# Kernel optimization log

Measured on AMD Instinct MI355X. Metric: run time of the kernel, lower is better.

Reference implementation:

```python
import jax, jax.numpy as jnp
import numpy as np
import math

B, T, C = 8, 2048, 1024
DIM_ATT, DIM_FFN = 1024, 4096
N_LAYER, LAYER_ID = 12, 1
EPS = 1e-5


def setup_inputs() -> dict:
    key = jax.random.key(0)
    ks = jax.random.split(key, 16)

    # deterministic init constants per RWKV source
    r01 = LAYER_ID / (N_LAYER - 1)
    r1a0 = 1.0 - LAYER_ID / N_LAYER
    ddd = (np.arange(C, dtype=np.float32) / C)[None, None, :]
    decay_speed = -5.0 + 8.0 * (np.arange(DIM_ATT, dtype=np.float32) / (DIM_ATT - 1)) ** (0.7 + 1.3 * r01)
    zigzag = (np.array([(i + 1) % 3 - 1 for i in range(DIM_ATT)], dtype=np.float32)) * 0.5

    def lin(k, out_d, in_d):
        return jax.random.normal(k, (out_d, in_d), jnp.float32) * (1.0 / math.sqrt(in_d))

    return {
        "x": jax.random.normal(ks[0], (B, T, C), jnp.float32),
        "ln1_w": jnp.ones((C,), jnp.float32),
        "ln1_b": jnp.zeros((C,), jnp.float32),
        "ln2_w": jnp.ones((C,), jnp.float32),
        "ln2_b": jnp.zeros((C,), jnp.float32),
        # time-mix (attention) params
        "att_tmk": jnp.asarray(ddd ** r1a0),
        "att_tmv": jnp.asarray(ddd ** r1a0 + 0.3 * r01),
        "att_tmr": jnp.asarray(ddd ** (0.5 * r1a0)),
        "time_decay": jnp.asarray(decay_speed),
        "time_first": jnp.asarray(np.full(DIM_ATT, math.log(0.3), np.float32) + zigzag),
        "Wk": lin(ks[1], DIM_ATT, C),
        "Wv": lin(ks[2], DIM_ATT, C),
        "Wr": lin(ks[3], DIM_ATT, C),
        "Wo": lin(ks[4], C, DIM_ATT),
        # channel-mix params
        "ffn_tmk": jnp.asarray(ddd ** r1a0),
        "ffn_tmr": jnp.asarray(ddd ** r1a0),
        "Wkey": lin(ks[5], DIM_FFN, C),
        "Wrec": lin(ks[6], C, C),
        "Wval": lin(ks[7], C, DIM_FFN),
    }


def layer_norm(x, w, b):
    mu = jnp.mean(x, axis=-1, keepdims=True)
    var = jnp.mean(jnp.square(x - mu), axis=-1, keepdims=True)
    return (x - mu) * jax.lax.rsqrt(var + EPS) * w + b


def time_shift(x):
    # xx[:, t] = x[:, t-1], zero at t=0  (nn.ZeroPad2d((0,0,1,-1)))
    return jnp.pad(x, ((0, 0), (1, 0), (0, 0)))[:, :-1, :]


def wkv(time_decay, time_first, k, v):
    # numerically stable RWKV-4 WKV recurrence, vectorized over (B, C)
    w = -jnp.exp(time_decay)  # [C]
    u = time_first            # [C]

    def step(carry, kv_t):
        aa, bb, pp = carry        # each [B, C]
        kt, vt = kv_t             # [B, C]
        ww = u + kt
        qq = jnp.maximum(pp, ww)
        e1 = jnp.exp(pp - qq)
        e2 = jnp.exp(ww - qq)
        y = (e1 * aa + e2 * vt) / (e1 * bb + e2)
        ww2 = pp + w
        qq2 = jnp.maximum(ww2, kt)
        e1b = jnp.exp(ww2 - qq2)
        e2b = jnp.exp(kt - qq2)
        return (e1b * aa + e2b * vt, e1b * bb + e2b, qq2), y

    init = (jnp.zeros_like(k[:, 0]), jnp.zeros_like(k[:, 0]),
            jnp.full_like(k[:, 0], -1e38))
    kT = jnp.swapaxes(k, 0, 1)  # [T, B, C]
    vT = jnp.swapaxes(v, 0, 1)
    _, yT = jax.lax.scan(step, init, (kT, vT))
    return jnp.swapaxes(yT, 0, 1)  # [B, T, C]


def reference(x, ln1_w, ln1_b, ln2_w, ln2_b,
              att_tmk, att_tmv, att_tmr, time_decay, time_first,
              Wk, Wv, Wr, Wo,
              ffn_tmk, ffn_tmr, Wkey, Wrec, Wval):
    # --- time-mix (attention) with residual ---
    h = layer_norm(x, ln1_w, ln1_b)
    hh = time_shift(h)
    xk = h * att_tmk + hh * (1 - att_tmk)
    xv = h * att_tmv + hh * (1 - att_tmv)
    xr = h * att_tmr + hh * (1 - att_tmr)
    k = xk @ Wk.T
    v = xv @ Wv.T
    sr = jax.nn.sigmoid(xr @ Wr.T)
    rwkv = sr * wkv(time_decay, time_first, k, v)
    x = x + rwkv @ Wo.T

    # --- channel-mix (FFN) with residual ---
    h = layer_norm(x, ln2_w, ln2_b)
    hh = time_shift(h)
    xk = h * ffn_tmk + hh * (1 - ffn_tmk)
    xr = h * ffn_tmr + hh * (1 - ffn_tmr)
    kk = jnp.square(jax.nn.relu(xk @ Wkey.T))
    kv = kk @ Wval.T
    x = x + jax.nn.sigmoid(xr @ Wrec.T) * kv
    return x
```

## Files before the change

### kernel.cpp

```cpp
#include <hip/hip_runtime.h>
#include <stdint.h>

#define B_ 8
#define T_ 2048
#define C_ 1024
#define F_ 4096
#define M_ (B_*T_)
#define NC 16
#define LCH (T_/NC)

typedef __attribute__((ext_vector_type(8))) short bf16x8;
typedef __attribute__((ext_vector_type(4))) float f32x4;

static __device__ __forceinline__ unsigned short f2bf(float f) {
    union { float f; unsigned u; } v; v.f = f;
    unsigned r = v.u + 0x7fffu + ((v.u >> 16) & 1u);
    return (unsigned short)(r >> 16);
}
static __device__ __forceinline__ float bf2f(unsigned short h) {
    union { unsigned u; float f; } v; v.u = ((unsigned)h) << 16;
    return v.f;
}

#define GLDS16(gp, lp) __builtin_amdgcn_global_load_lds( \
    (const __attribute__((address_space(1))) unsigned int*)(gp), \
    (__attribute__((address_space(3))) unsigned int*)(lp), 16, 0, 0)

#define SB0() __builtin_amdgcn_sched_barrier(0)
#define MFMA_BF16(a, b, c) __builtin_amdgcn_mfma_f32_16x16x32_bf16((a), (b), (c), 0, 0, 0)

struct WSrc { const float* p[7]; };

__global__ __launch_bounds__(256) void k_convert(WSrc w, unsigned short* __restrict__ dst) {
    size_t e = ((size_t)blockIdx.x * 256 + threadIdx.x) * 4;
    int seg = (int)(e >> 20);
    const float* s; size_t off;
    if (seg < 5)      { s = w.p[seg]; off = e - ((size_t)seg << 20); }
    else if (seg < 9) { s = w.p[5];   off = e - (5ull << 20); }
    else              { s = w.p[6];   off = e - (9ull << 20); }
    float4 v = *(const float4*)(s + off);
    ushort4 o;
    o.x = f2bf(v.x); o.y = f2bf(v.y); o.z = f2bf(v.z); o.w = f2bf(v.w);
    *(ushort4*)(dst + e) = o;
}

template<int THREE>
__global__ __launch_bounds__(256) void k_ln_mix(
    const float* __restrict__ xin, const float* __restrict__ lw, const float* __restrict__ lb,
    const float* __restrict__ tk, const float* __restrict__ tv, const float* __restrict__ tr,
    unsigned short* __restrict__ ok, unsigned short* __restrict__ ov, unsigned short* __restrict__ orr)
{
    __shared__ float sred[4][4];
    const int m = blockIdx.x;
    const int t = m & (T_ - 1);
    const int tid = threadIdx.x;
    const int col0 = tid * 4;

    const float4 xc = *(const float4*)(xin + (size_t)m * C_ + col0);
    float4 xp = make_float4(0.f, 0.f, 0.f, 0.f);
    if (t > 0) xp = *(const float4*)(xin + (size_t)(m - 1) * C_ + col0);

    float s1 = xc.x + xc.y + xc.z + xc.w;
    float s2 = xc.x*xc.x + xc.y*xc.y + xc.z*xc.z + xc.w*xc.w;
    float s3 = xp.x + xp.y + xp.z + xp.w;
    float s4 = xp.x*xp.x + xp.y*xp.y + xp.z*xp.z + xp.w*xp.w;
    #pragma unroll
    for (int off = 32; off > 0; off >>= 1) {
        s1 += __shfl_down(s1, off);
        s2 += __shfl_down(s2, off);
        s3 += __shfl_down(s3, off);
        s4 += __shfl_down(s4, off);
    }
    const int wave = tid >> 6, lane = tid & 63;
    if (lane == 0) { sred[0][wave]=s1; sred[1][wave]=s2; sred[2][wave]=s3; sred[3][wave]=s4; }
    __syncthreads();
    const float S1 = sred[0][0]+sred[0][1]+sred[0][2]+sred[0][3];
    const float S2 = sred[1][0]+sred[1][1]+sred[1][2]+sred[1][3];
    const float S3 = sred[2][0]+sred[2][1]+sred[2][2]+sred[2][3];
    const float S4 = sred[3][0]+sred[3][1]+sred[3][2]+sred[3][3];

    const float inv = 1.0f / (float)C_;
    const float muc = S1 * inv;
    const float rc  = rsqrtf(S2 * inv - muc * muc + 1e-5f);
    const float mup = S3 * inv;
    const float rp  = rsqrtf(S4 * inv - mup * mup + 1e-5f);

    const float xcv[4] = {xc.x, xc.y, xc.z, xc.w};
    const float xpv[4] = {xp.x, xp.y, xp.z, xp.w};
    unsigned short rk[4], rv[4], rr[4];
    #pragma unroll
    for (int i = 0; i < 4; ++i) {
        const int col = col0 + i;
        const float w_ = lw[col], b_ = lb[col];
        const float h  = (xcv[i] - muc) * rc * w_ + b_;
        const float hh = (t > 0) ? (xpv[i] - mup) * rp * w_ + b_ : 0.f;
        const float ak = tk[col];
        rk[i] = f2bf(h * ak + hh * (1.f - ak));
        if (THREE) { const float av = tv[col]; rv[i] = f2bf(h * av + hh * (1.f - av)); }
        const float ar = tr[col];
        rr[i] = f2bf(h * ar + hh * (1.f - ar));
    }
    const size_t o = (size_t)m * C_ + col0;
    ushort4 u;
    u.x = rk[0]; u.y = rk[1]; u.z = rk[2]; u.w = rk[3];
    *(ushort4*)(ok + o) = u;
    if (THREE) {
        u.x = rv[0]; u.y = rv[1]; u.z = rv[2]; u.w = rv[3];
        *(ushort4*)(ov + o) = u;
    }
    u.x = rr[0]; u.y = rr[1]; u.z = rr[2]; u.w = rr[3];
    *(ushort4*)(orr + o) = u;
}

__global__ __launch_bounds__(256) void k_wkv_local(
    const unsigned short* __restrict__ kb, const unsigned short* __restrict__ vb,
    const float* __restrict__ tdec, float4* __restrict__ st)
{
    const int g = blockIdx.x * 256 + threadIdx.x;
    const int c = g & (C_ - 1);
    const int j = (g >> 10) & (NC - 1);
    const int b = g >> 14;
    const float w = -__expf(tdec[c]);
    float aa = 0.f, bb = 0.f, pp = -1e38f;
    const size_t base = ((size_t)(b * T_ + j * LCH)) * C_ + c;
    #pragma unroll 4
    for (int t = 0; t < LCH; ++t) {
        const float kt = bf2f(kb[base + (size_t)t * C_]);
        const float vt = bf2f(vb[base + (size_t)t * C_]);
        const float ww2 = pp + w;
        const float qq2 = fmaxf(ww2, kt);
        const float e1b = __expf(ww2 - qq2);
        const float e2b = __expf(kt - qq2);
        aa = e1b * aa + e2b * vt;
        bb = e1b * bb + e2b;
        pp = qq2;
    }
    st[((size_t)b * NC + j) * C_ + c] = make_float4(aa, bb, pp, 0.f);
}

__global__ __launch_bounds__(256) void k_wkv_scan(
    const unsigned short* __restrict__ kb, const unsigned short* __restrict__ vb,
    const unsigned short* __restrict__ sr,
    const float* __restrict__ tdec, const float* __restrict__ tfirst,
    const float4* __restrict__ st, unsigned short* __restrict__ p)
{
    const int g = blockIdx.x * 256 + threadIdx.x;
    const int c = g & (C_ - 1);
    const int j = (g >> 10) & (NC - 1);
    const int b = g >> 14;
    const float w = -__expf(tdec[c]);
    const float u = tfirst[c];

    float aa = 0.f, bb = 0.f, pp = -1e38f;
    for (int i = 0; i < j; ++i) {
        const float4 s = st[((size_t)b * NC + i) * C_ + c];
        const float pdec = pp + w * (float)LCH;
        const float q  = fmaxf(pdec, s.z);
        const float eA = __expf(pdec - q);
        const float eB = __expf(s.z - q);
        aa = eA * aa + eB * s.x;
        bb = eA * bb + eB * s.y;
        pp = q;
    }

    const size_t base = ((size_t)(b * T_ + j * LCH)) * C_ + c;
    #pragma unroll 4
    for (int t = 0; t < LCH; ++t) {
        const size_t idx = base + (size_t)t * C_;
        const float kt = bf2f(kb[idx]);
        const float vt = bf2f(vb[idx]);
        const float ww = u + kt;
        const float qq = fmaxf(pp, ww);
        const float e1 = __expf(pp - qq);
        const float e2 = __expf(ww - qq);
        const float y  = (e1 * aa + e2 * vt) / (e1 * bb + e2);
        p[idx] = f2bf(bf2f(sr[idx]) * y);
        const float ww2 = pp + w;
        const float qq2 = fmaxf(ww2, kt);
        const float e1b = __expf(ww2 - qq2);
        const float e2b = __expf(kt - qq2);
        aa = e1b * aa + e2b * vt;
        bb = e1b * bb + e2b;
        pp = qq2;
    }
}

static __device__ __forceinline__ void gemm_core256(
    const unsigned short* __restrict__ A, int lda,
    const unsigned short* __restrict__ Bw, int ldb,
    int K, int m0, int n0,
    unsigned short* As, unsigned short* Bs, f32x4 acc[8][4])
{
    const int tid  = threadIdx.x;
    const int l    = tid & 63;
    const int l16  = l & 15, quad = l >> 4;
    const int w    = tid >> 6;
    const int wm   = w >> 2, wn = w & 3;

    const int sr_ = tid >> 3;
    const int sb_ = (tid & 7) ^ (sr_ & 7);
    const unsigned short* gA = A  + (size_t)(m0 + sr_) * lda + sb_ * 8;
    const unsigned short* gB = Bw + (size_t)(n0 + sr_) * ldb + sb_ * 8;

    auto stA = [&](int tt, int ss, int u) {
        GLDS16(gA + (size_t)u * 64 * lda + tt * 64, As + ss * 16384 + u * 4096 + w * 512);
    };
    auto stB = [&](int tt, int ss, int u) {
        GLDS16(gB + (size_t)u * 64 * ldb + tt * 64, Bs + ss * 16384 + u * 4096 + w * 512);
    };

    const int swz = l16 & 7;
    const unsigned short* aR = As + (wm * 128 + l16) * 64;
    const unsigned short* bR = Bs + (wn * 64  + l16) * 64;
    const int o0 = ((0 + quad) ^ swz) * 8;
    const int o1 = ((4 + quad) ^ swz) * 8;

    stA(0, 0, 0); stA(0, 0, 2);
    stB(0, 0, 0); stB(0, 0, 1); stB(0, 0, 2); stB(0, 0, 3);
    stA(0, 0, 1); stA(0, 0, 3);
    asm volatile("s_waitcnt vmcnt(0)" ::: "memory");
    SB0();
    __builtin_amdgcn_s_barrier();
    SB0();

    const int NT = K >> 6;
    for (int t = 0; t < NT; ++t) {
        const int rs = t & 1, ns = rs ^ 1;
        const unsigned short* ab = aR + rs * 16384;
        const unsigned short* bb = bR + rs * 16384;
        const bool pf = (t + 1 < NT);
        bf16x8 b0[4], b1[4];

        {
            bf16x8 a0[2], a1[2];
            #pragma unroll
            for (int j = 0; j < 4; ++j) {
                b0[j] = *(const bf16x8*)(bb + j * 1024 + o0);
                b1[j] = *(const bf16x8*)(bb + j * 1024 + o1);
            }
            #pragma unroll
            for (int i = 0; i < 2; ++i) {
                a0[i] = *(const bf16x8*)(ab + i * 1024 + o0);
                a1[i] = *(const bf16x8*)(ab + i * 1024 + o1);
            }
            if (pf) { stA(t + 1, ns, 0); stA(t + 1, ns, 2); }
            SB0();
            __builtin_amdgcn_s_barrier();
            asm volatile("s_waitcnt lgkmcnt(0)" ::: "memory");
            SB0();
            __builtin_amdgcn_s_setprio(1);
            #pragma unroll
            for (int i = 0; i < 2; ++i)
                #pragma unroll
                for (int j = 0; j < 4; ++j) {
                    acc[i][j] = MFMA_BF16(a0[i], b0[j], acc[i][j]);
                    acc[i][j] = MFMA_BF16(a1[i], b1[j], acc[i][j]);
                }
            __builtin_amdgcn_s_setprio(0);
            SB0();
            __builtin_amdgcn_s_barrier();
            SB0();
        }

        {
            bf16x8 a0[2], a1[2];
            #pragma unroll
            for (int i = 0; i < 2; ++i) {
                a0[i] = *(const bf16x8*)(ab + (2 + i) * 1024 + o0);
                a1[i] = *(const bf16x8*)(ab + (2 + i) * 1024 + o1);
            }
            if (pf) { stB(t + 1, ns, 0); stB(t + 1, ns, 1); stB(t + 1, ns, 2); stB(t + 1, ns, 3); }
            SB0();
            __builtin_amdgcn_s_barrier();
            asm volatile("s_waitcnt lgkmcnt(0)" ::: "memory");
            SB0();
            __builtin_amdgcn_s_setprio(1);
            #pragma unroll
            for (int i = 0; i < 2; ++i)
                #pragma unroll
                for (int j = 0; j < 4; ++j) {
                    acc[2 + i][j] = MFMA_BF16(a0[i], b0[j], acc[2 + i][j]);
                    acc[2 + i][j] = MFMA_BF16(a1[i], b1[j], acc[2 + i][j]);
                }
            __builtin_amdgcn_s_setprio(0);
            asm volatile("s_waitcnt vmcnt(6)" ::: "memory");
            SB0();
            __builtin_amdgcn_s_barrier();
            SB0();
        }

        {
            bf16x8 a0[2], a1[2];
            #pragma unroll
            for (int i = 0; i < 2; ++i) {
                a0[i] = *(const bf16x8*)(ab + (4 + i) * 1024 + o0);
                a1[i] = *(const bf16x8*)(ab + (4 + i) * 1024 + o1);
            }
            if (pf) { stA(t + 1, ns, 1); stA(t + 1, ns, 3); }
            SB0();
            __builtin_amdgcn_s_barrier();
            asm volatile("s_waitcnt lgkmcnt(0)" ::: "memory");
            SB0();
            __builtin_amdgcn_s_setprio(1);
            #pragma unroll
            for (int i = 0; i < 2; ++i)
                #pragma unroll
                for (int j = 0; j < 4; ++j) {
                    acc[4 + i][j] = MFMA_BF16(a0[i], b0[j], acc[4 + i][j]);
                    acc[4 + i][j] = MFMA_BF16(a1[i], b1[j], acc[4 + i][j]);
                }
            __builtin_amdgcn_s_setprio(0);
            SB0();
            __builtin_amdgcn_s_barrier();
            SB0();
        }

        {
            bf16x8 a0[2], a1[2];
            #pragma unroll
            for (int i = 0; i < 2; ++i) {
                a0[i] = *(const bf16x8*)(ab + (6 + i) * 1024 + o0);
                a1[i] = *(const bf16x8*)(ab + (6 + i) * 1024 + o1);
            }
            SB0();
            __builtin_amdgcn_s_barrier();
            asm volatile("s_waitcnt lgkmcnt(0)" ::: "memory");
            SB0();
            __builtin_amdgcn_s_setprio(1);
            #pragma unroll
            for (int i = 0; i < 2; ++i)
                #pragma unroll
                for (int j = 0; j < 4; ++j) {
                    acc[6 + i][j] = MFMA_BF16(a0[i], b0[j], acc[6 + i][j]);
                    acc[6 + i][j] = MFMA_BF16(a1[i], b1[j], acc[6 + i][j]);
                }
            __builtin_amdgcn_s_setprio(0);
            asm volatile("s_waitcnt vmcnt(2)" ::: "memory");
            SB0();
            __builtin_amdgcn_s_barrier();
            SB0();
        }
    }
}

template<int EPI>
__global__ __launch_bounds__(512, 1) void k_gemm(
    const unsigned short* __restrict__ A, int lda,
    const unsigned short* __restrict__ Bw, int ldb,
    int K, int N,
    float* __restrict__ outF, unsigned short* __restrict__ outH,
    const float* __restrict__ resid, const unsigned short* __restrict__ mul)
{
    __shared__ unsigned short As[2 * 16384];
    __shared__ unsigned short Bs[2 * 16384];
    f32x4 acc[8][4];
    const f32x4 zero = {0.f, 0.f, 0.f, 0.f};
    #pragma unroll
    for (int i = 0; i < 8; ++i)
        #pragma unroll
        for (int j = 0; j < 4; ++j) acc[i][j] = zero;

    const int m0 = blockIdx.x * 256, n0 = blockIdx.y * 256;
    gemm_core256(A, lda, Bw, ldb, K, m0, n0, As, Bs, acc);

    const int lane = threadIdx.x & 63, wave = threadIdx.x >> 6;
    const int quad = lane >> 4, l16 = lane & 15;
    const int wm = (wave >> 2) * 128, wn = (wave & 3) * 64;
    #pragma unroll
    for (int i = 0; i < 8; ++i) {
        const int rowb = m0 + wm + i * 16 + quad * 4;
        #pragma unroll
        for (int j = 0; j < 4; ++j) {
            const int col = n0 + wn + j * 16 + l16;
            #pragma unroll
            for (int r = 0; r < 4; ++r) {
                const size_t idx = (size_t)(rowb + r) * N + col;
                const float v = acc[i][j][r];
                if (EPI == 1)      outH[idx] = f2bf(1.f / (1.f + __expf(-v)));
                else if (EPI == 2) outF[idx] = resid[idx] + v;
                else if (EPI == 3) { const float z = v > 0.f ? v : 0.f; outH[idx] = f2bf(z * z); }
                else               outF[idx] = outF[idx] + bf2f(mul[idx]) * v;
            }
        }
    }
}

__global__ __launch_bounds__(512, 1) void k_gemm_kvr(
    const unsigned short* __restrict__ xk, const unsigned short* __restrict__ xv,
    const unsigned short* __restrict__ xr,
    const unsigned short* __restrict__ W3,
    unsigned short* __restrict__ ok, unsigned short* __restrict__ ov,
    unsigned short* __restrict__ orr)
{
    __shared__ unsigned short As[2 * 16384];
    __shared__ unsigned short Bs[2 * 16384];
    f32x4 acc[8][4];
    const f32x4 zero = {0.f, 0.f, 0.f, 0.f};
    #pragma unroll
    for (int i = 0; i < 8; ++i)
        #pragma unroll
        for (int j = 0; j < 4; ++j) acc[i][j] = zero;

    const int m0 = blockIdx.x * 256, n0 = blockIdx.y * 256;
    const int seg = n0 >> 10;
    const unsigned short* A = (seg == 0) ? xk : (seg == 1) ? xv : xr;
    unsigned short* outH    = (seg == 0) ? ok : (seg == 1) ? ov : orr;

    gemm_core256(A, C_, W3, C_, C_, m0, n0, As, Bs, acc);

    const int nl0 = n0 & (C_ - 1);
    const int lane = threadIdx.x & 63, wave = threadIdx.x >> 6;
    const int quad = lane >> 4, l16 = lane & 15;
    const int wm = (wave >> 2) * 128, wn = (wave & 3) * 64;
    #pragma unroll
    for (int i = 0; i < 8; ++i) {
        const int rowb = m0 + wm + i * 16 + quad * 4;
        #pragma unroll
        for (int j = 0; j < 4; ++j) {
            const int col = nl0 + wn + j * 16 + l16;
            #pragma unroll
            for (int r = 0; r < 4; ++r) {
                const size_t idx = (size_t)(rowb + r) * C_ + col;
                float v = acc[i][j][r];
                if (seg == 2) v = 1.f / (1.f + __expf(-v));
                outH[idx] = f2bf(v);
            }
        }
    }
}

extern "C" void kernel_launch(void* const* d_in, const int* in_sizes, int n_in,
                              void* d_out, int out_size, void* d_ws, size_t ws_size,
                              hipStream_t stream)
{
    const float* x      = (const float*)d_in[0];
    const float* ln1w   = (const float*)d_in[1];
    const float* ln1b   = (const float*)d_in[2];
    const float* ln2w   = (const float*)d_in[3];
    const float* ln2b   = (const float*)d_in[4];
    const float* atk    = (const float*)d_in[5];
    const float* atv    = (const float*)d_in[6];
    const float* atr    = (const float*)d_in[7];
    const float* tdec   = (const float*)d_in[8];
    const float* tfirst = (const float*)d_in[9];
    const float* Wk     = (const float*)d_in[10];
    const float* Wv     = (const float*)d_in[11];
    const float* Wr     = (const float*)d_in[12];
    const float* Wo     = (const float*)d_in[13];
    const float* ftk    = (const float*)d_in[14];
    const float* ftr    = (const float*)d_in[15];
    const float* Wkey   = (const float*)d_in[16];
    const float* Wrec   = (const float*)d_in[17];
    const float* Wval   = (const float*)d_in[18];
    float* out = (float*)d_out;

    char* ws = (char*)d_ws;
    const size_t MB = 1ull << 20;
    unsigned short* xk  = (unsigned short*)(ws + 0 * MB);
    unsigned short* xv  = (unsigned short*)(ws + 32 * MB);
    unsigned short* xr  = (unsigned short*)(ws + 64 * MB);
    unsigned short* sr  = (unsigned short*)(ws + 96 * MB);
    unsigned short* wb  = (unsigned short*)(ws + 128 * MB);
    float4* states      = (float4*)(ws + 0 * MB);
    unsigned short* p   = xv;
    unsigned short* xk2 = xk;
    unsigned short* xr2 = xr;
    unsigned short* s2  = sr;
    unsigned short* tmp = xv;
    unsigned short* kb  = (unsigned short*)d_out;
    unsigned short* vb  = (unsigned short*)d_out + (32*MB/2);

    unsigned short* W3_b   = wb;
    unsigned short* Wo_b   = wb + 3 * (1u << 20);
    unsigned short* Wrec_b = wb + 4 * (1u << 20);
    unsigned short* Wkey_b = wb + 5 * (1u << 20);
    unsigned short* Wval_b = wb + 9 * (1u << 20);

    WSrc wsrc; wsrc.p[0]=Wk; wsrc.p[1]=Wv; wsrc.p[2]=Wr; wsrc.p[3]=Wo;
    wsrc.p[4]=Wrec; wsrc.p[5]=Wkey; wsrc.p[6]=Wval;
    k_convert<<<dim3(13312), dim3(256), 0, stream>>>(wsrc, wb);

    k_ln_mix<1><<<dim3(M_), dim3(256), 0, stream>>>(x, ln1w, ln1b, atk, atv, atr, xk, xv, xr);

    k_gemm_kvr<<<dim3(64, 12), dim3(512), 0, stream>>>(xk, xv, xr, W3_b, kb, vb, sr);

    k_wkv_local<<<dim3(512), dim3(256), 0, stream>>>(kb, vb, tdec, states);
    k_wkv_scan<<<dim3(512), dim3(256), 0, stream>>>(kb, vb, sr, tdec, tfirst, states, p);

    k_gemm<2><<<dim3(64, 4), dim3(512), 0, stream>>>(p, 1024, Wo_b, 1024, 1024, 1024, out, (unsigned short*)nullptr, x, (const unsigned short*)nullptr);

    k_ln_mix<0><<<dim3(M_), dim3(256), 0, stream>>>(out, ln2w, ln2b, ftk, (const float*)nullptr, ftr, xk2, (unsigned short*)nullptr, xr2);

    k_gemm<1><<<dim3(64, 4), dim3(512), 0, stream>>>(xr2, 1024, Wrec_b, 1024, 1024, 1024, (float*)nullptr, s2, (const float*)nullptr, (const unsigned short*)nullptr);

    for (int f = 0; f < 4; ++f) {
        const unsigned short* WkeyF = Wkey_b + (size_t)f * 1024 * 1024;
        const unsigned short* WvalF = Wval_b + (size_t)f * 1024;
        k_gemm<3><<<dim3(64, 4), dim3(512), 0, stream>>>(xk2, 1024, WkeyF, 1024, 1024, 1024, (float*)nullptr, tmp, (const float*)nullptr, (const unsigned short*)nullptr);
        k_gemm<4><<<dim3(64, 4), dim3(512), 0, stream>>>(tmp, 1024, WvalF, 4096, 1024, 1024, out, (unsigned short*)nullptr, (const float*)nullptr, s2);
    }
}
```

Measured before the change: 943.3 us.

## Remove per-phase barriers in GEMM K-loop and double-buffer A register fragments

The bf16 MFMA GEMM main loop used to split each 64-wide K step into four phases, each with its own workgroup barriers. It now runs the four phases with a single barrier at the end of the K step. LDS reads for the next A fragments alternate between two register sets and are issued before the current phase's MFMAs, with partial lgkmcnt waits so LDS reads overlap MFMA work. All A prefetches for the next stage are issued in phase one and all B prefetches in phase two, then one vmcnt(0) wait runs at the end. This cuts synchronization overhead, but it uses more registers and gives less fine-grained interleaving of global-to-LDS traffic.

New measurement: 962.6 us. 2.1% more time.

```diff
diff --git a/kernel.cpp b/kernel.cpp
--- a/kernel.cpp
+++ b/kernel.cpp
@@ -215,9 +215,8 @@
     const int o0 = ((0 + quad) ^ swz) * 8;
     const int o1 = ((4 + quad) ^ swz) * 8;
 
-    stA(0, 0, 0); stA(0, 0, 2);
+    stA(0, 0, 0); stA(0, 0, 1); stA(0, 0, 2); stA(0, 0, 3);
     stB(0, 0, 0); stB(0, 0, 1); stB(0, 0, 2); stB(0, 0, 3);
-    stA(0, 0, 1); stA(0, 0, 3);
     asm volatile("s_waitcnt vmcnt(0)" ::: "memory");
     SB0();
     __builtin_amdgcn_s_barrier();
@@ -229,117 +228,91 @@
         const unsigned short* ab = aR + rs * 16384;
         const unsigned short* bb = bR + rs * 16384;
         const bool pf = (t + 1 < NT);
-        bf16x8 b0[4], b1[4];
-
-        {
-            bf16x8 a0[2], a1[2];
+        bf16x8 bc0[4], bc1[4], aP0[2], aP1[2], aQ0[2], aQ1[2];
+
+        #pragma unroll
+        for (int j = 0; j < 4; ++j) {
+            bc0[j] = *(const bf16x8*)(bb + j * 1024 + o0);
+            bc1[j] = *(const bf16x8*)(bb + j * 1024 + o1);
+        }
+        #pragma unroll
+        for (int r = 0; r < 2; ++r) {
+            aP0[r] = *(const bf16x8*)(ab + r * 1024 + o0);
+            aP1[r] = *(const bf16x8*)(ab + r * 1024 + o1);
+        }
+        SB0();
+        #pragma unroll
+        for (int r = 0; r < 2; ++r) {
+            aQ0[r] = *(const bf16x8*)(ab + (2 + r) * 1024 + o0);
+            aQ1[r] = *(const bf16x8*)(ab + (2 + r) * 1024 + o1);
+        }
+        if (pf) { stA(t + 1, ns, 0); stA(t + 1, ns, 1); stA(t + 1, ns, 2); stA(t + 1, ns, 3); }
+        asm volatile("s_waitcnt lgkmcnt(4)" ::: "memory");
+        SB0();
+        __builtin_amdgcn_s_setprio(1);
+        #pragma unroll
+        for (int r = 0; r < 2; ++r)
             #pragma unroll
             for (int j = 0; j < 4; ++j) {
-                b0[j] = *(const bf16x8*)(bb + j * 1024 + o0);
-                b1[j] = *(const bf16x8*)(bb + j * 1024 + o1);
-            }
-            #pragma unroll
-            for (int i = 0; i < 2; ++i) {
-                a0[i] = *(const bf16x8*)(ab + i * 1024 + o0);
-                a1[i] = *(const bf16x8*)(ab + i * 1024 + o1);
-            }
-            if (pf) { stA(t + 1, ns, 0); stA(t + 1, ns, 2); }
-            SB0();
-            __builtin_amdgcn_s_barrier();
-            asm volatile("s_waitcnt lgkmcnt(0)" ::: "memory");
-            SB0();
-            __builtin_amdgcn_s_setprio(1);
-            #pragma unroll
-            for (int i = 0; i < 2; ++i)
-                #pragma unroll
-                for (int j = 0; j < 4; ++j) {
-                    acc[i][j] = MFMA_BF16(a0[i], b0[j], acc[i][j]);
-                    acc[i][j] = MFMA_BF16(a1[i], b1[j], acc[i][j]);
-                }
-            __builtin_amdgcn_s_setprio(0);
-            SB0();
-            __builtin_amdgcn_s_barrier();
-            SB0();
-        }
-
-        {
-            bf16x8 a0[2], a1[2];
-            #pragma unroll
-            for (int i = 0; i < 2; ++i) {
-                a0[i] = *(const bf16x8*)(ab + (2 + i) * 1024 + o0);
-                a1[i] = *(const bf16x8*)(ab + (2 + i) * 1024 + o1);
-            }
-            if (pf) { stB(t + 1, ns, 0); stB(t + 1, ns, 1); stB(t + 1, ns, 2); stB(t + 1, ns, 3); }
-            SB0();
-            __builtin_amdgcn_s_barrier();
-            asm volatile("s_waitcnt lgkmcnt(0)" ::: "memory");
-            SB0();
-            __builtin_amdgcn_s_setprio(1);
-            #pragma unroll
-            for (int i = 0; i < 2; ++i)
-                #pragma unroll
-                for (int j = 0; j < 4; ++j) {
-                    acc[2 + i][j] = MFMA_BF16(a0[i], b0[j], acc[2 + i][j]);
-                    acc[2 + i][j] = MFMA_BF16(a1[i], b1[j], acc[2 + i][j]);
-                }
-            __builtin_amdgcn_s_setprio(0);
-            asm volatile("s_waitcnt vmcnt(6)" ::: "memory");
-            SB0();
-            __builtin_amdgcn_s_barrier();
-            SB0();
-        }
-
-        {
-            bf16x8 a0[2], a1[2];
-            #pragma unroll
-            for (int i = 0; i < 2; ++i) {
-                a0[i] = *(const bf16x8*)(ab + (4 + i) * 1024 + o0);
-                a1[i] = *(const bf16x8*)(ab + (4 + i) * 1024 + o1);
-            }
-            if (pf) { stA(t + 1, ns, 1); stA(t + 1, ns, 3); }
-            SB0();
-            __builtin_amdgcn_s_barrier();
-            asm volatile("s_waitcnt lgkmcnt(0)" ::: "memory");
-            SB0();
-            __builtin_amdgcn_s_setprio(1);
-            #pragma unroll
-            for (int i = 0; i < 2; ++i)
-                #pragma unroll
-                for (int j = 0; j < 4; ++j) {
-                    acc[4 + i][j] = MFMA_BF16(a0[i], b0[j], acc[4 + i][j]);
-                    acc[4 + i][j] = MFMA_BF16(a1[i], b1[j], acc[4 + i][j]);
-                }
-            __builtin_amdgcn_s_setprio(0);
-            SB0();
-            __builtin_amdgcn_s_barrier();
-            SB0();
-        }
-
-        {
-            bf16x8 a0[2], a1[2];
-            #pragma unroll
-            for (int i = 0; i < 2; ++i) {
-                a0[i] = *(const bf16x8*)(ab + (6 + i) * 1024 + o0);
-                a1[i] = *(const bf16x8*)(ab + (6 + i) * 1024 + o1);
-            }
-            SB0();
-            __builtin_amdgcn_s_barrier();
-            asm volatile("s_waitcnt lgkmcnt(0)" ::: "memory");
-            SB0();
-            __builtin_amdgcn_s_setprio(1);
-            #pragma unroll
-            for (int i = 0; i < 2; ++i)
-                #pragma unroll
-                for (int j = 0; j < 4; ++j) {
-                    acc[6 + i][j] = MFMA_BF16(a0[i], b0[j], acc[6 + i][j]);
-                    acc[6 + i][j] = MFMA_BF16(a1[i], b1[j], acc[6 + i][j]);
-                }
-            __builtin_amdgcn_s_setprio(0);
-            asm volatile("s_waitcnt vmcnt(2)" ::: "memory");
-            SB0();
-            __builtin_amdgcn_s_barrier();
-            SB0();
-        }
+                acc[r][j] = MFMA_BF16(aP0[r], bc0[j], acc[r][j]);
+                acc[r][j] = MFMA_BF16(aP1[r], bc1[j], acc[r][j]);
+            }
+        __builtin_amdgcn_s_setprio(0);
+        SB0();
+
+        #pragma unroll
+        for (int r = 0; r < 2; ++r) {
+            aP0[r] = *(const bf16x8*)(ab + (4 + r) * 1024 + o0);
+            aP1[r] = *(const bf16x8*)(ab + (4 + r) * 1024 + o1);
+        }
+        if (pf) { stB(t + 1, ns, 0); stB(t + 1, ns, 1); stB(t + 1, ns, 2); stB(t + 1, ns, 3); }
+        asm volatile("s_waitcnt lgkmcnt(4)" ::: "memory");
+        SB0();
+        __builtin_amdgcn_s_setprio(1);
+        #pragma unroll
+        for (int r = 0; r < 2; ++r)
+            #pragma unroll
+            for (int j = 0; j < 4; ++j) {
+                acc[2 + r][j] = MFMA_BF16(aQ0[r], bc0[j], acc[2 + r][j]);
+                acc[2 + r][j] = MFMA_BF16(aQ1[r], bc1[j], acc[2 + r][j]);
+            }
+        __builtin_amdgcn_s_setprio(0);
+        SB0();
+
+        #pragma unroll
+        for (int r = 0; r < 2; ++r) {
+            aQ0[r] = *(const bf16x8*)(ab + (6 + r) * 1024 + o0);
+            aQ1[r] = *(const bf16x8*)(ab + (6 + r) * 1024 + o1);
+        }
+        asm volatile("s_waitcnt lgkmcnt(4)" ::: "memory");
+        SB0();
+        __builtin_amdgcn_s_setprio(1);
+        #pragma unroll
+        for (int r = 0; r < 2; ++r)
+            #pragma unroll
+            for (int j = 0; j < 4; ++j) {
+                acc[4 + r][j] = MFMA_BF16(aP0[r], bc0[j], acc[4 + r][j]);
+                acc[4 + r][j] = MFMA_BF16(aP1[r], bc1[j], acc[4 + r][j]);
+            }
+        __builtin_amdgcn_s_setprio(0);
+        SB0();
+
+        asm volatile("s_waitcnt lgkmcnt(0)" ::: "memory");
+        SB0();
+        __builtin_amdgcn_s_setprio(1);
+        #pragma unroll
+        for (int r = 0; r < 2; ++r)
+            #pragma unroll
+            for (int j = 0; j < 4; ++j) {
+                acc[6 + r][j] = MFMA_BF16(aQ0[r], bc0[j], acc[6 + r][j]);
+                acc[6 + r][j] = MFMA_BF16(aQ1[r], bc1[j], acc[6 + r][j]);
+            }
+        __builtin_amdgcn_s_setprio(0);
+        SB0();
+        asm volatile("s_waitcnt vmcnt(0)" ::: "memory");
+        SB0();
+        __builtin_amdgcn_s_barrier();
+        SB0();
     }
 }
 
```
